# Optimization experiments

Measured on AMD Instinct MI355X. Metric: run time of the kernel, lower is better.

The kernel has to match this reference:

```python
import jax, jax.numpy as jnp
import numpy as np

NUM_HEADS = 4
EMBED_DIM = 256
HEAD_DIM = EMBED_DIM // NUM_HEADS
B, N = 4, 4096


def setup_inputs() -> dict:
    key = jax.random.key(0)
    kq, kk, kv, kw = jax.random.split(key, 4)
    q = jax.random.normal(kq, (B, N, EMBED_DIM), dtype=jnp.float32)
    k = jax.random.normal(kk, (B, N, EMBED_DIM), dtype=jnp.float32)
    v = jax.random.normal(kv, (B, N, EMBED_DIM), dtype=jnp.float32)
    W_out = jax.random.normal(kw, (EMBED_DIM, EMBED_DIM), dtype=jnp.float32) * (1.0 / np.sqrt(EMBED_DIM))
    b_out = jnp.zeros((EMBED_DIM,), dtype=jnp.float32)
    return {"q": q, "k": k, "v": v, "W_out": W_out, "b_out": b_out}


def reference(q, k, v, W_out, b_out):
    b, n, _ = q.shape
    # [b, n, e] -> [b, h, n, d]
    qh = q.reshape(b, n, NUM_HEADS, HEAD_DIM).transpose(0, 2, 1, 3)
    kh = k.reshape(b, n, NUM_HEADS, HEAD_DIM).transpose(0, 2, 1, 3)
    vh = v.reshape(b, n, NUM_HEADS, HEAD_DIM).transpose(0, 2, 1, 3)
    scale = 1.0 / jnp.sqrt(jnp.asarray(HEAD_DIM, dtype=qh.dtype))
    # full [b, h, n, n] score matrix, as in the original module
    attn = jnp.einsum('bhqd,bhkd->bhqk', qh, kh) * scale
    attn = jax.nn.softmax(attn, axis=-1)
    out = jnp.einsum('bhqk,bhkd->bhqd', attn, vh)
    out = out.transpose(0, 2, 1, 3).reshape(b, n, EMBED_DIM)
    # nn.Linear: x @ W.T + b
    return out @ W_out.T + b_out
```

## Files before the change

### kernel.cpp

```cpp
#include <hip/hip_runtime.h>
#include <hip/hip_bf16.h>

#define B_ 4
#define H_ 4
#define N_ 4096
#define D_ 64
#define E_ 256
#define KVB 64
#define QBLK 128
#define NT (N_ / KVB)

typedef short short8 __attribute__((ext_vector_type(8)));
typedef float f32x4 __attribute__((ext_vector_type(4)));
typedef float f32x16 __attribute__((ext_vector_type(16)));

__device__ __forceinline__ ushort f2bf(float f) {
  union { float f; unsigned u; } a; a.f = f;
  unsigned r = a.u + 0x7fffu + ((a.u >> 16) & 1u);
  return (ushort)(r >> 16);
}

__device__ __forceinline__ uint4 pack8(float a0, float a1, float a2, float a3,
                                       float a4, float a5, float a6, float a7) {
  uint4 u;
  u.x = (unsigned)f2bf(a0) | ((unsigned)f2bf(a1) << 16);
  u.y = (unsigned)f2bf(a2) | ((unsigned)f2bf(a3) << 16);
  u.z = (unsigned)f2bf(a4) | ((unsigned)f2bf(a5) << 16);
  u.w = (unsigned)f2bf(a6) | ((unsigned)f2bf(a7) << 16);
  return u;
}

__device__ __forceinline__ unsigned cvt_pk_bf16(float lo, float hi) {
  unsigned r;
  asm("v_cvt_pk_bf16_f32 %0, %1, %2" : "=v"(r) : "v"(lo), "v"(hi));
  return r;
}

__device__ __forceinline__ void permlane32_swap(unsigned &a, unsigned &b) {
  asm volatile("v_permlane32_swap_b32 %0, %1" : "+v"(a), "+v"(b));
}

__device__ __forceinline__ void gload16(const void* g, void* l) {
  __builtin_amdgcn_global_load_lds(
      (const __attribute__((address_space(1))) void*)g,
      (__attribute__((address_space(3))) void*)l, 16, 0, 0);
}

__global__ void cast_w_kernel(const float* __restrict__ W, ushort* __restrict__ Wb) {
  int i = blockIdx.x * blockDim.x + threadIdx.x;
  float4 x = ((const float4*)W)[i];
  ushort4 o;
  o.x = f2bf(x.x); o.y = f2bf(x.y); o.z = f2bf(x.z); o.w = f2bf(x.w);
  ((ushort4*)Wb)[i] = o;
}

__global__ void prep_kv(const float* __restrict__ k, const float* __restrict__ v,
                        ushort* __restrict__ Kb, ushort* __restrict__ Vtb) {
  __shared__ float kt[64][65];
  __shared__ float vt[64][65];
  const int gid = blockIdx.x;
  const int bh = gid >> 6, t = gid & 63;
  const int b = bh >> 2, h = bh & 3;
  const int tid = threadIdx.x;
  const int rr = tid >> 4, cc = (tid & 15) * 4;
  const float* kg = k + ((size_t)b * N_ + t * 64) * E_ + h * 64;
  const float* vg = v + ((size_t)b * N_ + t * 64) * E_ + h * 64;
  ushort* ko = Kb + (size_t)gid * 4096;
  ushort* vo = Vtb + (size_t)gid * 4096;

  for (int it = 0; it < 4; ++it) {
    int r = rr + it * 16;
    float4 kx = *(const float4*)(kg + (size_t)r * E_ + cc);
    float4 vx = *(const float4*)(vg + (size_t)r * E_ + cc);
    kt[r][cc] = kx.x; kt[r][cc + 1] = kx.y; kt[r][cc + 2] = kx.z; kt[r][cc + 3] = kx.w;
    vt[r][cc] = vx.x; vt[r][cc + 1] = vx.y; vt[r][cc + 2] = vx.z; vt[r][cc + 3] = vx.w;
  }
  __syncthreads();

  for (int j = 0; j < 2; ++j) {
    int u = j * 256 + tid;
    int frag = u >> 6, l = u & 63;
    int a = (frag >> 2) * 32 + (l & 31);
    int c0 = (frag & 3) * 16 + ((l >> 5) & 1) * 8;
    *(uint4*)(ko + u * 8) = pack8(kt[a][c0], kt[a][c0 + 1], kt[a][c0 + 2], kt[a][c0 + 3],
                                  kt[a][c0 + 4], kt[a][c0 + 5], kt[a][c0 + 6], kt[a][c0 + 7]);
    *(uint4*)(vo + u * 8) = pack8(vt[c0][a], vt[c0 + 1][a], vt[c0 + 2][a], vt[c0 + 3][a],
                                  vt[c0 + 4][a], vt[c0 + 5][a], vt[c0 + 6][a], vt[c0 + 7][a]);
  }
}

__launch_bounds__(256, 2)
__global__ void attn_kernel(const float* __restrict__ q,
                            const ushort* __restrict__ Kb,
                            const ushort* __restrict__ Vtb,
                            ushort* __restrict__ X) {
  __shared__ __attribute__((aligned(16))) ushort SM[2][2][4096];
  __shared__ float Lb[2][2][32];
  __shared__ float Lb2[2][2][32];

  const int bid = blockIdx.x;
  const int swz = (bid & 7) * 64 + (bid >> 3);
  const int bh = swz >> 5;
  const int qt = swz & 31;
  const int b = bh >> 2, h = bh & 3;
  const int tid = threadIdx.x;
  const int wid = tid >> 6;
  const int wq = wid & 1;
  const int kh = wid >> 1;
  const int lane = tid & 63;
  const int ln = lane & 31;
  const int hi = lane >> 5;

  const char* Kg = (const char*)Kb + (size_t)bh * NT * 8192;
  const char* Vg = (const char*)Vtb + (size_t)bh * NT * 8192;

  const int wsl = wid * 1024;
  const int gsl = wsl + lane * 16;

  const float SC = 0.125f * 1.44269504f;
  const int qrow0 = qt * QBLK + wq * 64;
  short8 qf[2][4];
#pragma unroll
  for (int qg = 0; qg < 2; ++qg) {
    const float* Qg = q + ((size_t)b * N_ + qrow0 + qg * 32 + ln) * E_ + h * D_;
#pragma unroll
    for (int ks = 0; ks < 4; ++ks) {
      const float* p = Qg + ks * 16 + hi * 8;
      float4 x0 = *(const float4*)(p);
      float4 x1 = *(const float4*)(p + 4);
      short8 f;
      f[0] = (short)f2bf(x0.x * SC); f[1] = (short)f2bf(x0.y * SC);
      f[2] = (short)f2bf(x0.z * SC); f[3] = (short)f2bf(x0.w * SC);
      f[4] = (short)f2bf(x1.x * SC); f[5] = (short)f2bf(x1.y * SC);
      f[6] = (short)f2bf(x1.z * SC); f[7] = (short)f2bf(x1.w * SC);
      qf[qg][ks] = f;
    }
  }

  f32x16 O00 = (f32x16)0.0f, O01 = (f32x16)0.0f;
  f32x16 O10 = (f32x16)0.0f, O11 = (f32x16)0.0f;
  float lsum0 = 0.f, lsum1 = 0.f;

  gload16(Kg + gsl,        (char*)&SM[0][0][0] + wsl);
  gload16(Kg + 4096 + gsl, (char*)&SM[0][0][0] + 4096 + wsl);
  gload16(Vg + gsl,        (char*)&SM[0][1][0] + wsl);
  gload16(Vg + 4096 + gsl, (char*)&SM[0][1][0] + 4096 + wsl);
  asm volatile("s_waitcnt vmcnt(0)" ::: "memory");
  __builtin_amdgcn_sched_barrier(0);
  __syncthreads();
  int cur = 0;

  for (int t = 0; t < NT; ++t) {
    if (t + 1 < NT) {
      const char* kg = Kg + (size_t)(t + 1) * 8192;
      const char* vg = Vg + (size_t)(t + 1) * 8192;
      gload16(kg + gsl,        (char*)&SM[cur ^ 1][0][0] + wsl);
      gload16(kg + 4096 + gsl, (char*)&SM[cur ^ 1][0][0] + 4096 + wsl);
      gload16(vg + gsl,        (char*)&SM[cur ^ 1][1][0] + wsl);
      gload16(vg + 4096 + gsl, (char*)&SM[cur ^ 1][1][0] + 4096 + wsl);
    }

    const char* Kl = (const char*)&SM[cur][0][0];
    const char* Vl = (const char*)&SM[cur][1][0];

    short8 kf[4];
#pragma unroll
    for (int ks = 0; ks < 4; ++ks)
      kf[ks] = *(short8*)(Kl + (kh * 4 + ks) * 1024 + lane * 16);

    f32x16 S0 = (f32x16)0.0f, S1 = (f32x16)0.0f;
    __builtin_amdgcn_s_setprio(1);
#pragma unroll
    for (int ks = 0; ks < 4; ++ks) {
      S0 = __builtin_amdgcn_mfma_f32_32x32x16_bf16(kf[ks], qf[0][ks], S0, 0, 0, 0);
      S1 = __builtin_amdgcn_mfma_f32_32x32x16_bf16(kf[ks], qf[1][ks], S1, 0, 0, 0);
    }
    __builtin_amdgcn_s_setprio(0);

    short8 vf[2][2];
#pragma unroll
    for (int db = 0; db < 2; ++db)
#pragma unroll
      for (int s = 0; s < 2; ++s)
        vf[db][s] = *(short8*)(Vl + (db * 4 + kh * 2 + s) * 1024 + lane * 16);

    float p0[16], p1[16];
#pragma unroll
    for (int i = 0; i < 16; ++i) {
      p0[i] = __builtin_amdgcn_exp2f(S0[i]);
      p1[i] = __builtin_amdgcn_exp2f(S1[i]);
    }
    {
      float s1[8];
#pragma unroll
      for (int i = 0; i < 8; ++i) s1[i] = p0[2 * i] + p0[2 * i + 1];
#pragma unroll
      for (int i = 0; i < 4; ++i) s1[i] = s1[2 * i] + s1[2 * i + 1];
      lsum0 += (s1[0] + s1[1]) + (s1[2] + s1[3]);
#pragma unroll
      for (int i = 0; i < 8; ++i) s1[i] = p1[2 * i] + p1[2 * i + 1];
#pragma unroll
      for (int i = 0; i < 4; ++i) s1[i] = s1[2 * i] + s1[2 * i + 1];
      lsum1 += (s1[0] + s1[1]) + (s1[2] + s1[3]);
    }

    short8 pa0[2], pa1[2];
#pragma unroll
    for (int s = 0; s < 2; ++s) {
      int base = s * 8;
      {
        unsigned w0 = cvt_pk_bf16(p0[base + 0], p0[base + 1]);
        unsigned w2 = cvt_pk_bf16(p0[base + 4], p0[base + 5]);
        permlane32_swap(w0, w2);
        unsigned w1 = cvt_pk_bf16(p0[base + 2], p0[base + 3]);
        unsigned w3 = cvt_pk_bf16(p0[base + 6], p0[base + 7]);
        permlane32_swap(w1, w3);
        uint4 u; u.x = w0; u.y = w1; u.z = w2; u.w = w3;
        union { uint4 u4; short8 s8; } cv; cv.u4 = u;
        pa0[s] = cv.s8;
      }
      {
        unsigned w0 = cvt_pk_bf16(p1[base + 0], p1[base + 1]);
        unsigned w2 = cvt_pk_bf16(p1[base + 4], p1[base + 5]);
        permlane32_swap(w0, w2);
        unsigned w1 = cvt_pk_bf16(p1[base + 2], p1[base + 3]);
        unsigned w3 = cvt_pk_bf16(p1[base + 6], p1[base + 7]);
        permlane32_swap(w1, w3);
        uint4 u; u.x = w0; u.y = w1; u.z = w2; u.w = w3;
        union { uint4 u4; short8 s8; } cv; cv.u4 = u;
        pa1[s] = cv.s8;
      }
    }

    __builtin_amdgcn_s_setprio(1);
#pragma unroll
    for (int s = 0; s < 2; ++s) {
      O00 = __builtin_amdgcn_mfma_f32_32x32x16_bf16(pa0[s], vf[0][s], O00, 0, 0, 0);
      O01 = __builtin_amdgcn_mfma_f32_32x32x16_bf16(pa0[s], vf[1][s], O01, 0, 0, 0);
      O10 = __builtin_amdgcn_mfma_f32_32x32x16_bf16(pa1[s], vf[0][s], O10, 0, 0, 0);
      O11 = __builtin_amdgcn_mfma_f32_32x32x16_bf16(pa1[s], vf[1][s], O11, 0, 0, 0);
    }
    __builtin_amdgcn_s_setprio(0);

    asm volatile("s_waitcnt vmcnt(0)" ::: "memory");
    __builtin_amdgcn_sched_barrier(0);
    __syncthreads();
    cur ^= 1;
  }

  float l0 = lsum0 + __shfl_xor(lsum0, 32);
  float l1 = lsum1 + __shfl_xor(lsum1, 32);
  float* Ox = (float*)&SM[0][0][0];
  if (kh) {
    if (lane < 32) { Lb[wq][0][ln] = l0; Lb[wq][1][ln] = l1; }
#pragma unroll
    for (int r2 = 0; r2 < 16; ++r2) {
      Ox[wq * 4096 + 0 * 2048 + 0 * 1024 + r2 * 64 + lane] = O00[r2];
      Ox[wq * 4096 + 0 * 2048 + 1 * 1024 + r2 * 64 + lane] = O01[r2];
      Ox[wq * 4096 + 1 * 2048 + 0 * 1024 + r2 * 64 + lane] = O10[r2];
      Ox[wq * 4096 + 1 * 2048 + 1 * 1024 + r2 * 64 + lane] = O11[r2];
    }
  }
  __syncthreads();
  if (!kh) {
    float lt0 = l0 + Lb[wq][0][ln];
    float lt1 = l1 + Lb[wq][1][ln];
    if (lane < 32) { Lb2[wq][0][ln] = lt0; Lb2[wq][1][ln] = lt1; }
    asm volatile("" ::: "memory");
#pragma unroll
    for (int r2 = 0; r2 < 16; ++r2) {
      O00[r2] += Ox[wq * 4096 + 0 * 2048 + 0 * 1024 + r2 * 64 + lane];
      O01[r2] += Ox[wq * 4096 + 0 * 2048 + 1 * 1024 + r2 * 64 + lane];
      O10[r2] += Ox[wq * 4096 + 1 * 2048 + 0 * 1024 + r2 * 64 + lane];
      O11[r2] += Ox[wq * 4096 + 1 * 2048 + 1 * 1024 + r2 * 64 + lane];
    }
    ushort* Xp = X + ((size_t)b * N_) * E_ + h * D_;
#pragma unroll
    for (int r2 = 0; r2 < 16; ++r2) {
      int crow = (r2 & 3) + 8 * (r2 >> 2) + 4 * hi;
      float i0 = 1.0f / Lb2[wq][0][crow];
      float i1 = 1.0f / Lb2[wq][1][crow];
      int q0 = qrow0 + crow;
      int q1 = qrow0 + 32 + crow;
      Xp[(size_t)q0 * E_ + ln]      = f2bf(O00[r2] * i0);
      Xp[(size_t)q0 * E_ + 32 + ln] = f2bf(O01[r2] * i0);
      Xp[(size_t)q1 * E_ + ln]      = f2bf(O10[r2] * i1);
      Xp[(size_t)q1 * E_ + 32 + ln] = f2bf(O11[r2] * i1);
    }
  }
}

__launch_bounds__(256, 2)
__global__ void proj_kernel(const ushort* __restrict__ X, const ushort* __restrict__ Wb,
                            const float* __restrict__ bias, float* __restrict__ out) {
  const int m0   = blockIdx.x * 64;
  const int tid  = threadIdx.x;
  const int wid  = tid >> 6;
  const int lane = tid & 63;
  const int g    = lane >> 4;
  const int lr   = lane & 15;
  const int n0   = wid * 64;

  f32x4 acc[4][4];
  for (int mb = 0; mb < 4; ++mb)
    for (int nb = 0; nb < 4; ++nb)
      acc[mb][nb] = (f32x4){0.f, 0.f, 0.f, 0.f};

  for (int k0 = 0; k0 < E_; k0 += 32) {
    short8 af[4], bfr[4];
    for (int mb = 0; mb < 4; ++mb)
      af[mb] = *(const short8*)(X + (size_t)(m0 + mb * 16 + lr) * E_ + k0 + g * 8);
    for (int nb = 0; nb < 4; ++nb)
      bfr[nb] = *(const short8*)(Wb + (size_t)(n0 + nb * 16 + lr) * E_ + k0 + g * 8);
    for (int mb = 0; mb < 4; ++mb)
      for (int nb = 0; nb < 4; ++nb)
        acc[mb][nb] = __builtin_amdgcn_mfma_f32_16x16x32_bf16(af[mb], bfr[nb], acc[mb][nb], 0, 0, 0);
  }

  for (int nb = 0; nb < 4; ++nb) {
    float bv = bias[n0 + nb * 16 + lr];
    for (int mb = 0; mb < 4; ++mb)
      for (int r = 0; r < 4; ++r)
        out[(size_t)(m0 + mb * 16 + g * 4 + r) * E_ + n0 + nb * 16 + lr] = acc[mb][nb][r] + bv;
  }
}

extern "C" void kernel_launch(void* const* d_in, const int* in_sizes, int n_in,
                              void* d_out, int out_size, void* d_ws, size_t ws_size,
                              hipStream_t stream) {
  const float* q    = (const float*)d_in[0];
  const float* k    = (const float*)d_in[1];
  const float* v    = (const float*)d_in[2];
  const float* W    = (const float*)d_in[3];
  const float* bias = (const float*)d_in[4];

  char* ws = (char*)d_ws;
  ushort* X   = (ushort*)ws;
  ushort* Wb  = (ushort*)(ws + 8388608);
  ushort* Kb  = (ushort*)(ws + 8388608 + 131072);
  ushort* Vtb = (ushort*)(ws + 8388608 + 131072 + 8388608);

  cast_w_kernel<<<64, 256, 0, stream>>>(W, Wb);
  prep_kv<<<B_ * H_ * NT, 256, 0, stream>>>(k, v, Kb, Vtb);
  attn_kernel<<<B_ * H_ * (N_ / QBLK), 256, 0, stream>>>(q, Kb, Vtb, X);
  proj_kernel<<<(B_ * N_) / 64, 256, 0, stream>>>(X, Wb, bias, (float*)d_out);
}
```

Baseline: 111.8 us.

## Give each wave private K/V LDS buffers and drop per-tile block barriers

Each wave now loads only the K and V fragments it consumes into its own double-buffered LDS region, so the per-iteration __syncthreads is removed. Waves wait with a partial vmcnt so the next tile's loads stay in flight while the current tile is computed. Waves sharing the same kh now fetch duplicate K/V data, which raises global/L2 traffic, and LDS use doubles. This relies on wave-local visibility of the async LDS loads without a block barrier.

```diff
diff --git a/kernel.cpp b/kernel.cpp
--- a/kernel.cpp
+++ b/kernel.cpp
@@ -94,7 +94,7 @@
                             const ushort* __restrict__ Kb,
                             const ushort* __restrict__ Vtb,
                             ushort* __restrict__ X) {
-  __shared__ __attribute__((aligned(16))) ushort SM[2][2][4096];
+  __shared__ __attribute__((aligned(16))) ushort SM[4][2][2][2048];
   __shared__ float Lb[2][2][32];
   __shared__ float Lb2[2][2][32];
 
@@ -111,11 +111,13 @@
   const int ln = lane & 31;
   const int hi = lane >> 5;
 
-  const char* Kg = (const char*)Kb + (size_t)bh * NT * 8192;
-  const char* Vg = (const char*)Vtb + (size_t)bh * NT * 8192;
-
-  const int wsl = wid * 1024;
-  const int gsl = wsl + lane * 16;
+  const char* Kg = (const char*)Kb + (size_t)bh * NT * 8192 + kh * 4096 + lane * 16;
+  const char* Vg = (const char*)Vtb + (size_t)bh * NT * 8192 + kh * 2048 + lane * 16;
+
+  char* Kl0 = (char*)&SM[wid][0][0][0];
+  char* Vl0 = (char*)&SM[wid][0][1][0];
+  char* Kl1 = (char*)&SM[wid][1][0][0];
+  char* Vl1 = (char*)&SM[wid][1][1][0];
 
   const float SC = 0.125f * 1.44269504f;
   const int qrow0 = qt * QBLK + wq * 64;
@@ -141,32 +143,40 @@
   f32x16 O10 = (f32x16)0.0f, O11 = (f32x16)0.0f;
   float lsum0 = 0.f, lsum1 = 0.f;
 
-  gload16(Kg + gsl,        (char*)&SM[0][0][0] + wsl);
-  gload16(Kg + 4096 + gsl, (char*)&SM[0][0][0] + 4096 + wsl);
-  gload16(Vg + gsl,        (char*)&SM[0][1][0] + wsl);
-  gload16(Vg + 4096 + gsl, (char*)&SM[0][1][0] + 4096 + wsl);
+  auto STAGE = [&](char* Kl, char* Vl, int t) {
+    const char* kg = Kg + (size_t)t * 8192;
+    const char* vg = Vg + (size_t)t * 8192;
+#pragma unroll
+    for (int c = 0; c < 4; ++c)
+      gload16(kg + c * 1024, Kl + c * 1024);
+    gload16(vg,               Vl);
+    gload16(vg + 1024,        Vl + 1024);
+    gload16(vg + 4096,        Vl + 2048);
+    gload16(vg + 4096 + 1024, Vl + 3072);
+  };
+
+  STAGE(Kl0, Vl0, 0);
   asm volatile("s_waitcnt vmcnt(0)" ::: "memory");
   __builtin_amdgcn_sched_barrier(0);
-  __syncthreads();
-  int cur = 0;
 
   for (int t = 0; t < NT; ++t) {
+    const int curb = t & 1;
+    char* Klc = curb ? Kl1 : Kl0;
+    char* Vlc = curb ? Vl1 : Vl0;
+
     if (t + 1 < NT) {
-      const char* kg = Kg + (size_t)(t + 1) * 8192;
-      const char* vg = Vg + (size_t)(t + 1) * 8192;
-      gload16(kg + gsl,        (char*)&SM[cur ^ 1][0][0] + wsl);
-      gload16(kg + 4096 + gsl, (char*)&SM[cur ^ 1][0][0] + 4096 + wsl);
-      gload16(vg + gsl,        (char*)&SM[cur ^ 1][1][0] + wsl);
-      gload16(vg + 4096 + gsl, (char*)&SM[cur ^ 1][1][0] + 4096 + wsl);
-    }
-
-    const char* Kl = (const char*)&SM[cur][0][0];
-    const char* Vl = (const char*)&SM[cur][1][0];
+      STAGE(curb ? Kl0 : Kl1, curb ? Vl0 : Vl1, t + 1);
+      __builtin_amdgcn_sched_barrier(0);
+      asm volatile("s_waitcnt vmcnt(8)" ::: "memory");
+    } else {
+      asm volatile("s_waitcnt vmcnt(0)" ::: "memory");
+    }
+    __builtin_amdgcn_sched_barrier(0);
 
     short8 kf[4];
 #pragma unroll
     for (int ks = 0; ks < 4; ++ks)
-      kf[ks] = *(short8*)(Kl + (kh * 4 + ks) * 1024 + lane * 16);
+      kf[ks] = *(short8*)(Klc + ks * 1024 + lane * 16);
 
     f32x16 S0 = (f32x16)0.0f, S1 = (f32x16)0.0f;
     __builtin_amdgcn_s_setprio(1);
@@ -182,7 +192,7 @@
     for (int db = 0; db < 2; ++db)
 #pragma unroll
       for (int s = 0; s < 2; ++s)
-        vf[db][s] = *(short8*)(Vl + (db * 4 + kh * 2 + s) * 1024 + lane * 16);
+        vf[db][s] = *(short8*)(Vlc + (db * 2 + s) * 1024 + lane * 16);
 
     float p0[16], p1[16];
 #pragma unroll
@@ -242,15 +252,14 @@
     }
     __builtin_amdgcn_s_setprio(0);
 
-    asm volatile("s_waitcnt vmcnt(0)" ::: "memory");
     __builtin_amdgcn_sched_barrier(0);
-    __syncthreads();
-    cur ^= 1;
-  }
+  }
+
+  __syncthreads();
 
   float l0 = lsum0 + __shfl_xor(lsum0, 32);
   float l1 = lsum1 + __shfl_xor(lsum1, 32);
-  float* Ox = (float*)&SM[0][0][0];
+  float* Ox = (float*)&SM[0][0][0][0];
   if (kh) {
     if (lane < 32) { Lb[wq][0][ln] = l0; Lb[wq][1][ln] = l1; }
 #pragma unroll
```

After: 116.1 us. +3.8%, slower.
